# Kernel optimization log

Hardware: AMD Instinct MI355X
Metric: run time of the kernel (lower is better)

Reference implementation:

```python
import jax, jax.numpy as jnp
import numpy as np

N_NODES = 200000
D = 128            # in_channels
B_GRAPHS = 512     # batch_size
STEPS = 3          # processing_steps


def setup_inputs() -> dict:
    key = jax.random.key(0)
    k = jax.random.split(key, 6)
    x = jax.random.normal(k[0], (N_NODES, D), dtype=jnp.float32)
    batch = jnp.sort(jax.random.randint(k[1], (N_NODES,), 0, B_GRAPHS, dtype=jnp.int64))
    s = 0.1
    W_ih = jax.random.normal(k[2], (3 * D, 2 * D), dtype=jnp.float32) * s
    W_hh = jax.random.normal(k[3], (3 * D, D), dtype=jnp.float32) * s
    b_ih = jax.random.normal(k[4], (3 * D,), dtype=jnp.float32) * s
    b_hh = jax.random.normal(k[5], (3 * D,), dtype=jnp.float32) * s
    return {"x": x, "batch": batch, "batch_size": B_GRAPHS,
            "W_ih": W_ih, "W_hh": W_hh, "b_ih": b_ih, "b_hh": b_hh}


def _gru_cell(inp, h, W_ih, W_hh, b_ih, b_hh):
    # inp: [B, 2d], h: [B, d]; PyTorch GRU gate order: r, z, n
    gi = inp @ W_ih.T + b_ih  # [B, 3d]
    gh = h @ W_hh.T + b_hh    # [B, 3d]
    gi_r, gi_z, gi_n = jnp.split(gi, 3, axis=-1)
    gh_r, gh_z, gh_n = jnp.split(gh, 3, axis=-1)
    r = jax.nn.sigmoid(gi_r + gh_r)
    z = jax.nn.sigmoid(gi_z + gh_z)
    n = jnp.tanh(gi_n + r * gh_n)
    return (1.0 - z) * n + z * h


def reference(x, batch, batch_size, W_ih, W_hh, b_ih, b_hh):
    B = batch_size
    d = x.shape[1]
    h = jnp.zeros((B, d), dtype=x.dtype)
    q_star = jnp.zeros((B, 2 * d), dtype=x.dtype)
    for _ in range(STEPS):
        h = _gru_cell(q_star, h, W_ih, W_hh, b_ih, b_hh)
        q = h  # num_layers=1: output == new hidden state
        e = jnp.sum(x * q[batch], axis=-1)  # [N]
        m = jax.ops.segment_max(e, batch, num_segments=B)
        ex = jnp.exp(e - m[batch])
        s = jax.ops.segment_sum(ex, batch, num_segments=B)
        a = ex / (s[batch] + 1e-16)  # segment softmax weights [N]
        r = jax.ops.segment_sum(a[:, None] * x, batch, num_segments=B)  # [B, d]
        q_star = jnp.concatenate([q, r], axis=-1)
    return q_star
```

## Files before the change

### kernel.cpp

```cpp
#include <hip/hip_runtime.h>
#include <math.h>

constexpr int D = 128;
constexpr int B = 512;
constexpr int STEPS = 3;
constexpr int NW_IH = 3 * D * 2 * D;
constexpr int NW_HH = 3 * D * D;

__device__ __forceinline__ float sigmoidf_(float x) { return 1.f / (1.f + __expf(-x)); }
__device__ __forceinline__ float bflo(unsigned int u) { return __uint_as_float(u << 16); }
__device__ __forceinline__ float bfhi(unsigned int u) { return __uint_as_float(u & 0xffff0000u); }
__device__ __forceinline__ unsigned short f2bf_rn(float f) {
    unsigned int u = __float_as_uint(f);
    u += 0x7fffu + ((u >> 16) & 1u);
    return (unsigned short)(u >> 16);
}
__device__ __forceinline__ float4 ld4(const float* p) { return *(const float4*)p; }

__global__ __launch_bounds__(256) void k_prep(const float* __restrict__ Wih,
        const float* __restrict__ Whh, const int* __restrict__ batch, int n,
        unsigned short* __restrict__ wih_bf, unsigned short* __restrict__ whh_bf,
        int* __restrict__ seg) {
    int i = blockIdx.x * blockDim.x + threadIdx.x;
    if (i < NW_IH) wih_bf[i] = f2bf_rn(Wih[i]);
    else if (i < NW_IH + NW_HH) whh_bf[i - NW_IH] = f2bf_rn(Whh[i - NW_IH]);
    if (i <= B) {
        int lo = 0, hi = n;
        while (lo < hi) { int mid = (lo + hi) >> 1; if (batch[mid] < i) lo = mid + 1; else hi = mid; }
        seg[i] = lo;
    }
}

struct Trip { float4 a0, a1, b0, b1, c0, c1, d0, d1; };

__global__ __launch_bounds__(256, 2) void k_set2set(
        const float* __restrict__ x,
        const unsigned short* __restrict__ wih_bf,
        const unsigned short* __restrict__ whh_bf,
        const float* __restrict__ bih, const float* __restrict__ bhh,
        const int* __restrict__ seg, float* __restrict__ out) {
    __shared__ __align__(16) float s_q[2 * D];
    __shared__ __align__(16) float s_h[D];
    __shared__ float s_gi[3 * D], s_gh[3 * D];
    __shared__ float sm[16], sl[16];
    __shared__ __align__(16) float rpart[4][D];

    const int b = blockIdx.x;
    const int tid = threadIdx.x;
    const int start = seg[b], end = seg[b + 1];
    const int g = tid >> 4;
    const int s = tid & 15;

    if (tid < 2 * D) s_q[tid] = 0.f;
    if (tid < D) s_h[tid] = 0.f;
    __syncthreads();

    const int len = end - start;
    const int F = len >> 6;
    const float* xb = x + (size_t)(start + g) * D + s * 8;

    float m_run, l_run;
    float4 acc0, acc1;
    float4 q0, q1;

    auto load_trip = [&](Trip& T, int t) {
        const float* p = xb + (size_t)t * (64 * D);
        T.a0 = ld4(p);            T.a1 = ld4(p + 4);
        T.b0 = ld4(p + 16 * D);   T.b1 = ld4(p + 16 * D + 4);
        T.c0 = ld4(p + 32 * D);   T.c1 = ld4(p + 32 * D + 4);
        T.d0 = ld4(p + 48 * D);   T.d1 = ld4(p + 48 * D + 4);
    };
    auto dot8 = [&](const float4& lo, const float4& hi) {
        float p = lo.x * q0.x;
        p = fmaf(lo.y, q0.y, p); p = fmaf(lo.z, q0.z, p); p = fmaf(lo.w, q0.w, p);
        p = fmaf(hi.x, q1.x, p); p = fmaf(hi.y, q1.y, p);
        p = fmaf(hi.z, q1.z, p); p = fmaf(hi.w, q1.w, p);
        return p;
    };
    auto compute = [&](const Trip& T) {
        float p0 = dot8(T.a0, T.a1);
        float p1 = dot8(T.b0, T.b1);
        float p2 = dot8(T.c0, T.c1);
        float p3 = dot8(T.d0, T.d1);
        p0 += __shfl_xor(p0, 1, 64); p1 += __shfl_xor(p1, 1, 64);
        p2 += __shfl_xor(p2, 1, 64); p3 += __shfl_xor(p3, 1, 64);
        p0 += __shfl_xor(p0, 2, 64); p1 += __shfl_xor(p1, 2, 64);
        p2 += __shfl_xor(p2, 2, 64); p3 += __shfl_xor(p3, 2, 64);
        p0 += __shfl_xor(p0, 4, 64); p1 += __shfl_xor(p1, 4, 64);
        p2 += __shfl_xor(p2, 4, 64); p3 += __shfl_xor(p3, 4, 64);
        p0 += __shfl_xor(p0, 8, 64); p1 += __shfl_xor(p1, 8, 64);
        p2 += __shfl_xor(p2, 8, 64); p3 += __shfl_xor(p3, 8, 64);
        float nm = fmaxf(m_run, fmaxf(fmaxf(p0, p1), fmaxf(p2, p3)));
        float sc = __expf(m_run - nm);
        float e0 = __expf(p0 - nm), e1 = __expf(p1 - nm);
        float e2 = __expf(p2 - nm), e3 = __expf(p3 - nm);
        l_run = fmaf(l_run, sc, (e0 + e1) + (e2 + e3));
        acc0.x = fmaf(acc0.x, sc, fmaf(e0, T.a0.x, fmaf(e1, T.b0.x, fmaf(e2, T.c0.x, e3 * T.d0.x))));
        acc0.y = fmaf(acc0.y, sc, fmaf(e0, T.a0.y, fmaf(e1, T.b0.y, fmaf(e2, T.c0.y, e3 * T.d0.y))));
        acc0.z = fmaf(acc0.z, sc, fmaf(e0, T.a0.z, fmaf(e1, T.b0.z, fmaf(e2, T.c0.z, e3 * T.d0.z))));
        acc0.w = fmaf(acc0.w, sc, fmaf(e0, T.a0.w, fmaf(e1, T.b0.w, fmaf(e2, T.c0.w, e3 * T.d0.w))));
        acc1.x = fmaf(acc1.x, sc, fmaf(e0, T.a1.x, fmaf(e1, T.b1.x, fmaf(e2, T.c1.x, e3 * T.d1.x))));
        acc1.y = fmaf(acc1.y, sc, fmaf(e0, T.a1.y, fmaf(e1, T.b1.y, fmaf(e2, T.c1.y, e3 * T.d1.y))));
        acc1.z = fmaf(acc1.z, sc, fmaf(e0, T.a1.z, fmaf(e1, T.b1.z, fmaf(e2, T.c1.z, e3 * T.d1.z))));
        acc1.w = fmaf(acc1.w, sc, fmaf(e0, T.a1.w, fmaf(e1, T.b1.w, fmaf(e2, T.c1.w, e3 * T.d1.w))));
        m_run = nm;
    };
    auto one_node = [&](const float4& v0, const float4& v1) {
        float p = dot8(v0, v1);
        p += __shfl_xor(p, 1, 64);
        p += __shfl_xor(p, 2, 64);
        p += __shfl_xor(p, 4, 64);
        p += __shfl_xor(p, 8, 64);
        float nm = fmaxf(m_run, p);
        float sc = __expf(m_run - nm);
        float e  = __expf(p - nm);
        l_run = fmaf(l_run, sc, e);
        acc0.x = fmaf(acc0.x, sc, e * v0.x);
        acc0.y = fmaf(acc0.y, sc, e * v0.y);
        acc0.z = fmaf(acc0.z, sc, e * v0.z);
        acc0.w = fmaf(acc0.w, sc, e * v0.w);
        acc1.x = fmaf(acc1.x, sc, e * v1.x);
        acc1.y = fmaf(acc1.y, sc, e * v1.y);
        acc1.z = fmaf(acc1.z, sc, e * v1.z);
        acc1.w = fmaf(acc1.w, sc, e * v1.w);
        m_run = nm;
    };

    Trip A, Bv;

    for (int step = 0; step < STEPS; ++step) {
        if (F > 0) load_trip(A, 0);

        if (tid < 192) {
            const int r0 = tid * 2, r1 = r0 + 1;
            float gi0 = bih[r0], gi1 = bih[r1];
            float gh0 = bhh[r0], gh1 = bhh[r1];
            const float4* q4 = (const float4*)s_q;
            const float4* h4 = (const float4*)s_h;
            const uint4* w0 = (const uint4*)(wih_bf + (size_t)r0 * (2 * D));
            const uint4* w1 = (const uint4*)(wih_bf + (size_t)r1 * (2 * D));
#pragma unroll 4
            for (int c = 0; c < 32; ++c) {
                uint4 wa = w0[c], wb = w1[c];
                float4 qa = q4[2 * c], qb = q4[2 * c + 1];
                gi0 = fmaf(bflo(wa.x), qa.x, gi0); gi0 = fmaf(bfhi(wa.x), qa.y, gi0);
                gi0 = fmaf(bflo(wa.y), qa.z, gi0); gi0 = fmaf(bfhi(wa.y), qa.w, gi0);
                gi0 = fmaf(bflo(wa.z), qb.x, gi0); gi0 = fmaf(bfhi(wa.z), qb.y, gi0);
                gi0 = fmaf(bflo(wa.w), qb.z, gi0); gi0 = fmaf(bfhi(wa.w), qb.w, gi0);
                gi1 = fmaf(bflo(wb.x), qa.x, gi1); gi1 = fmaf(bfhi(wb.x), qa.y, gi1);
                gi1 = fmaf(bflo(wb.y), qa.z, gi1); gi1 = fmaf(bfhi(wb.y), qa.w, gi1);
                gi1 = fmaf(bflo(wb.z), qb.x, gi1); gi1 = fmaf(bfhi(wb.z), qb.y, gi1);
                gi1 = fmaf(bflo(wb.w), qb.z, gi1); gi1 = fmaf(bfhi(wb.w), qb.w, gi1);
            }
            const uint4* v0 = (const uint4*)(whh_bf + (size_t)r0 * D);
            const uint4* v1 = (const uint4*)(whh_bf + (size_t)r1 * D);
#pragma unroll 4
            for (int c = 0; c < 16; ++c) {
                uint4 wa = v0[c], wb = v1[c];
                float4 ha = h4[2 * c], hb = h4[2 * c + 1];
                gh0 = fmaf(bflo(wa.x), ha.x, gh0); gh0 = fmaf(bfhi(wa.x), ha.y, gh0);
                gh0 = fmaf(bflo(wa.y), ha.z, gh0); gh0 = fmaf(bfhi(wa.y), ha.w, gh0);
                gh0 = fmaf(bflo(wa.z), hb.x, gh0); gh0 = fmaf(bfhi(wa.z), hb.y, gh0);
                gh0 = fmaf(bflo(wa.w), hb.z, gh0); gh0 = fmaf(bfhi(wa.w), hb.w, gh0);
                gh1 = fmaf(bflo(wb.x), ha.x, gh1); gh1 = fmaf(bfhi(wb.x), ha.y, gh1);
                gh1 = fmaf(bflo(wb.y), ha.z, gh1); gh1 = fmaf(bfhi(wb.y), ha.w, gh1);
                gh1 = fmaf(bflo(wb.z), hb.x, gh1); gh1 = fmaf(bfhi(wb.z), hb.y, gh1);
                gh1 = fmaf(bflo(wb.w), hb.z, gh1); gh1 = fmaf(bfhi(wb.w), hb.w, gh1);
            }
            s_gi[r0] = gi0; s_gi[r1] = gi1;
            s_gh[r0] = gh0; s_gh[r1] = gh1;
        }
        __syncthreads();
        if (tid < D) {
            const int t = tid;
            float r  = sigmoidf_(s_gi[t] + s_gh[t]);
            float z  = sigmoidf_(s_gi[D + t] + s_gh[D + t]);
            float nn = tanhf(s_gi[2 * D + t] + r * s_gh[2 * D + t]);
            float hn = (1.f - z) * nn + z * s_h[t];
            s_h[t] = hn;
            s_q[t] = hn;
        }
        __syncthreads();

        q0 = ((const float4*)s_h)[2 * s];
        q1 = ((const float4*)s_h)[2 * s + 1];
        m_run = -INFINITY; l_run = 0.f;
        acc0 = make_float4(0.f, 0.f, 0.f, 0.f);
        acc1 = make_float4(0.f, 0.f, 0.f, 0.f);

        if (F > 0) {
            int t = 0;
            for (; t + 2 < F; t += 2) {
                load_trip(Bv, t + 1); compute(A);
                load_trip(A,  t + 2); compute(Bv);
            }
            if (t + 2 == F) { load_trip(Bv, t + 1); compute(A); compute(Bv); }
            else            { compute(A); }
        }
        {
            const int nt = start + g + (F << 6);
#pragma unroll
            for (int u = 0; u < 4; ++u) {
                const int nd = nt + (u << 4);
                if (nd < end) {
                    const float* p = x + (size_t)nd * D + s * 8;
                    one_node(ld4(p), ld4(p + 4));
                }
            }
        }

        if (s == 0) { sm[g] = m_run; sl[g] = l_run; }
        __syncthreads();

        {
            const float mv = sm[s];
            const float lv = sl[s];
            float M = mv;
            M = fmaxf(M, __shfl_xor(M, 1, 64));
            M = fmaxf(M, __shfl_xor(M, 2, 64));
            M = fmaxf(M, __shfl_xor(M, 4, 64));
            M = fmaxf(M, __shfl_xor(M, 8, 64));
            float term = (mv == -INFINITY) ? 0.f : lv * __expf(mv - M);
            term += __shfl_xor(term, 1, 64);
            term += __shfl_xor(term, 2, 64);
            term += __shfl_xor(term, 4, 64);
            term += __shfl_xor(term, 8, 64);
            const float inv = 1.f / (term + 1e-16f);
            const float fac = (m_run == -INFINITY) ? 0.f : __expf(m_run - M) * inv;
            acc0.x *= fac; acc0.y *= fac; acc0.z *= fac; acc0.w *= fac;
            acc1.x *= fac; acc1.y *= fac; acc1.z *= fac; acc1.w *= fac;
        }
        acc0.x += __shfl_xor(acc0.x, 16, 64); acc0.y += __shfl_xor(acc0.y, 16, 64);
        acc0.z += __shfl_xor(acc0.z, 16, 64); acc0.w += __shfl_xor(acc0.w, 16, 64);
        acc1.x += __shfl_xor(acc1.x, 16, 64); acc1.y += __shfl_xor(acc1.y, 16, 64);
        acc1.z += __shfl_xor(acc1.z, 16, 64); acc1.w += __shfl_xor(acc1.w, 16, 64);
        acc0.x += __shfl_xor(acc0.x, 32, 64); acc0.y += __shfl_xor(acc0.y, 32, 64);
        acc0.z += __shfl_xor(acc0.z, 32, 64); acc0.w += __shfl_xor(acc0.w, 32, 64);
        acc1.x += __shfl_xor(acc1.x, 32, 64); acc1.y += __shfl_xor(acc1.y, 32, 64);
        acc1.z += __shfl_xor(acc1.z, 32, 64); acc1.w += __shfl_xor(acc1.w, 32, 64);

        const int wv = tid >> 6;
        if ((tid & 63) < 16) {
            float4* dst = (float4*)&rpart[wv][s * 8];
            dst[0] = acc0; dst[1] = acc1;
        }
        __syncthreads();
        if (tid < D) {
            float v = (rpart[0][tid] + rpart[1][tid]) + (rpart[2][tid] + rpart[3][tid]);
            s_q[D + tid] = v;
        }
        __syncthreads();
    }

    if (tid < 2 * D) out[(size_t)b * (2 * D) + tid] = s_q[tid];
}

extern "C" void kernel_launch(void* const* d_in, const int* in_sizes, int n_in,
                              void* d_out, int out_size, void* d_ws, size_t ws_size,
                              hipStream_t stream) {
    const float* x    = (const float*)d_in[0];
    const int*   batch= (const int*)d_in[1];
    const float* Wih  = (const float*)d_in[3];
    const float* Whh  = (const float*)d_in[4];
    const float* bih  = (const float*)d_in[5];
    const float* bhh  = (const float*)d_in[6];
    const int n = in_sizes[0] / D;

    char* ws = (char*)d_ws;
    int* seg = (int*)ws;
    unsigned short* wih_bf = (unsigned short*)(ws + 4096);
    unsigned short* whh_bf = (unsigned short*)(ws + 4096 + (size_t)NW_IH * 2);

    const int total = NW_IH + NW_HH;
    k_prep<<<(total + 255) / 256, 256, 0, stream>>>(Wih, Whh, batch, n, wih_bf, whh_bf, seg);
    k_set2set<<<B, 256, 0, stream>>>(x, wih_bf, whh_bf, bih, bhh, seg, (float*)d_out);
}
```

Before: 236.2 us.

## Deepen x prefetch to four trips and overlap next-step loads with reductions

The streaming loop now keeps four trips of x rows in registers instead of two, and handles the segment tail with clamped loads plus masking instead of a separate per-node loop. The first four trips for the next step are issued before the cross-group reduction and the GRU matvec, so their memory latency is hidden behind that work. A finite sentinel replaces -INFINITY so the special-case checks can be dropped. This costs many more live vector registers, which under launch_bounds(256,2) could cause spills or lower occupancy.

```diff
diff --git a/kernel.cpp b/kernel.cpp
--- a/kernel.cpp
+++ b/kernel.cpp
@@ -1,11 +1,13 @@
 #include <hip/hip_runtime.h>
 #include <math.h>
+#include <float.h>
 
 constexpr int D = 128;
 constexpr int B = 512;
 constexpr int STEPS = 3;
 constexpr int NW_IH = 3 * D * 2 * D;
 constexpr int NW_HH = 3 * D * D;
+constexpr float NEG_HUGE = -3.402823466e38f;
 
 __device__ __forceinline__ float sigmoidf_(float x) { return 1.f / (1.f + __expf(-x)); }
 __device__ __forceinline__ float bflo(unsigned int u) { return __uint_as_float(u << 16); }
@@ -16,6 +18,7 @@
     return (unsigned short)(u >> 16);
 }
 __device__ __forceinline__ float4 ld4(const float* p) { return *(const float4*)p; }
+__device__ __forceinline__ int imin_(int a, int b) { return a < b ? a : b; }
 
 __global__ __launch_bounds__(256) void k_prep(const float* __restrict__ Wih,
         const float* __restrict__ Whh, const int* __restrict__ batch, int n,
@@ -50,25 +53,28 @@
     const int start = seg[b], end = seg[b + 1];
     const int g = tid >> 4;
     const int s = tid & 15;
-
-    if (tid < 2 * D) s_q[tid] = 0.f;
-    if (tid < D) s_h[tid] = 0.f;
-    __syncthreads();
+    const int s8 = s * 8;
 
     const int len = end - start;
-    const int F = len >> 6;
-    const float* xb = x + (size_t)(start + g) * D + s * 8;
+    const int FT = (len + 63) >> 6;
+    const int gbase = start + g;
+    const int eclamp = (len > 0) ? end - 1 : start;
 
     float m_run, l_run;
     float4 acc0, acc1;
     float4 q0, q1;
+    Trip T0_, T1_, T2_, T3_;
 
     auto load_trip = [&](Trip& T, int t) {
-        const float* p = xb + (size_t)t * (64 * D);
-        T.a0 = ld4(p);            T.a1 = ld4(p + 4);
-        T.b0 = ld4(p + 16 * D);   T.b1 = ld4(p + 16 * D + 4);
-        T.c0 = ld4(p + 32 * D);   T.c1 = ld4(p + 32 * D + 4);
-        T.d0 = ld4(p + 48 * D);   T.d1 = ld4(p + 48 * D + 4);
+        const int n0 = gbase + (t << 6);
+        const float* p0 = x + ((size_t)imin_(n0,      eclamp) << 7) + s8;
+        const float* p1 = x + ((size_t)imin_(n0 + 16, eclamp) << 7) + s8;
+        const float* p2 = x + ((size_t)imin_(n0 + 32, eclamp) << 7) + s8;
+        const float* p3 = x + ((size_t)imin_(n0 + 48, eclamp) << 7) + s8;
+        T.a0 = ld4(p0); T.a1 = ld4(p0 + 4);
+        T.b0 = ld4(p1); T.b1 = ld4(p1 + 4);
+        T.c0 = ld4(p2); T.c1 = ld4(p2 + 4);
+        T.d0 = ld4(p3); T.d1 = ld4(p3 + 4);
     };
     auto dot8 = [&](const float4& lo, const float4& hi) {
         float p = lo.x * q0.x;
@@ -77,7 +83,7 @@
         p = fmaf(hi.z, q1.z, p); p = fmaf(hi.w, q1.w, p);
         return p;
     };
-    auto compute = [&](const Trip& T) {
+    auto compute_core = [&](const Trip& T, bool masked, int t) {
         float p0 = dot8(T.a0, T.a1);
         float p1 = dot8(T.b0, T.b1);
         float p2 = dot8(T.c0, T.c1);
@@ -90,10 +96,22 @@
         p2 += __shfl_xor(p2, 4, 64); p3 += __shfl_xor(p3, 4, 64);
         p0 += __shfl_xor(p0, 8, 64); p1 += __shfl_xor(p1, 8, 64);
         p2 += __shfl_xor(p2, 8, 64); p3 += __shfl_xor(p3, 8, 64);
-        float nm = fmaxf(m_run, fmaxf(fmaxf(p0, p1), fmaxf(p2, p3)));
+        bool m0 = true, m1 = true, m2 = true, m3 = true;
+        float h0 = p0, h1 = p1, h2 = p2, h3 = p3;
+        if (masked) {
+            const int n0 = gbase + (t << 6);
+            m0 = n0 < end; m1 = n0 + 16 < end; m2 = n0 + 32 < end; m3 = n0 + 48 < end;
+            h0 = m0 ? p0 : NEG_HUGE; h1 = m1 ? p1 : NEG_HUGE;
+            h2 = m2 ? p2 : NEG_HUGE; h3 = m3 ? p3 : NEG_HUGE;
+        }
+        float nm = fmaxf(m_run, fmaxf(fmaxf(h0, h1), fmaxf(h2, h3)));
         float sc = __expf(m_run - nm);
         float e0 = __expf(p0 - nm), e1 = __expf(p1 - nm);
         float e2 = __expf(p2 - nm), e3 = __expf(p3 - nm);
+        if (masked) {
+            e0 = m0 ? e0 : 0.f; e1 = m1 ? e1 : 0.f;
+            e2 = m2 ? e2 : 0.f; e3 = m3 ? e3 : 0.f;
+        }
         l_run = fmaf(l_run, sc, (e0 + e1) + (e2 + e3));
         acc0.x = fmaf(acc0.x, sc, fmaf(e0, T.a0.x, fmaf(e1, T.b0.x, fmaf(e2, T.c0.x, e3 * T.d0.x))));
         acc0.y = fmaf(acc0.y, sc, fmaf(e0, T.a0.y, fmaf(e1, T.b0.y, fmaf(e2, T.c0.y, e3 * T.d0.y))));
@@ -105,32 +123,19 @@
         acc1.w = fmaf(acc1.w, sc, fmaf(e0, T.a1.w, fmaf(e1, T.b1.w, fmaf(e2, T.c1.w, e3 * T.d1.w))));
         m_run = nm;
     };
-    auto one_node = [&](const float4& v0, const float4& v1) {
-        float p = dot8(v0, v1);
-        p += __shfl_xor(p, 1, 64);
-        p += __shfl_xor(p, 2, 64);
-        p += __shfl_xor(p, 4, 64);
-        p += __shfl_xor(p, 8, 64);
-        float nm = fmaxf(m_run, p);
-        float sc = __expf(m_run - nm);
-        float e  = __expf(p - nm);
-        l_run = fmaf(l_run, sc, e);
-        acc0.x = fmaf(acc0.x, sc, e * v0.x);
-        acc0.y = fmaf(acc0.y, sc, e * v0.y);
-        acc0.z = fmaf(acc0.z, sc, e * v0.z);
-        acc0.w = fmaf(acc0.w, sc, e * v0.w);
-        acc1.x = fmaf(acc1.x, sc, e * v1.x);
-        acc1.y = fmaf(acc1.y, sc, e * v1.y);
-        acc1.z = fmaf(acc1.z, sc, e * v1.z);
-        acc1.w = fmaf(acc1.w, sc, e * v1.w);
-        m_run = nm;
-    };
-
-    Trip A, Bv;
+    auto compute  = [&](const Trip& T)        { compute_core(T, false, 0); };
+    auto computeM = [&](const Trip& T, int t) { compute_core(T, true,  t); };
+
+    if (FT > 0) load_trip(T0_, 0);
+    if (FT > 1) load_trip(T1_, 1);
+    if (FT > 2) load_trip(T2_, 2);
+    if (FT > 3) load_trip(T3_, 3);
+
+    if (tid < 2 * D) s_q[tid] = 0.f;
+    if (tid < D) s_h[tid] = 0.f;
+    __syncthreads();
 
     for (int step = 0; step < STEPS; ++step) {
-        if (F > 0) load_trip(A, 0);
-
         if (tid < 192) {
             const int r0 = tid * 2, r1 = r0 + 1;
             float gi0 = bih[r0], gi1 = bih[r1];
@@ -184,29 +189,36 @@
 
         q0 = ((const float4*)s_h)[2 * s];
         q1 = ((const float4*)s_h)[2 * s + 1];
-        m_run = -INFINITY; l_run = 0.f;
+        m_run = NEG_HUGE; l_run = 0.f;
         acc0 = make_float4(0.f, 0.f, 0.f, 0.f);
         acc1 = make_float4(0.f, 0.f, 0.f, 0.f);
 
-        if (F > 0) {
-            int t = 0;
-            for (; t + 2 < F; t += 2) {
-                load_trip(Bv, t + 1); compute(A);
-                load_trip(A,  t + 2); compute(Bv);
-            }
-            if (t + 2 == F) { load_trip(Bv, t + 1); compute(A); compute(Bv); }
-            else            { compute(A); }
-        }
-        {
-            const int nt = start + g + (F << 6);
-#pragma unroll
-            for (int u = 0; u < 4; ++u) {
-                const int nd = nt + (u << 4);
-                if (nd < end) {
-                    const float* p = x + (size_t)nd * D + s * 8;
-                    one_node(ld4(p), ld4(p + 4));
-                }
-            }
+        int t = 0;
+        while (t + 8 <= FT) {
+            compute(T0_); load_trip(T0_, t + 4);
+            compute(T1_); load_trip(T1_, t + 5);
+            compute(T2_); load_trip(T2_, t + 6);
+            compute(T3_); load_trip(T3_, t + 7);
+            t += 4;
+        }
+        int rem = FT - t;
+        if (rem > 4) {
+            compute(T0_); load_trip(T0_, t + 4);
+            compute(T1_); if (rem > 5) load_trip(T1_, t + 5);
+            compute(T2_); if (rem > 6) load_trip(T2_, t + 6);
+            compute(T3_);
+            t += 4; rem -= 4;
+        }
+        if (rem > 0) { if (t     == FT - 1) computeM(T0_, t);     else compute(T0_); }
+        if (rem > 1) { if (t + 1 == FT - 1) computeM(T1_, t + 1); else compute(T1_); }
+        if (rem > 2) { if (t + 2 == FT - 1) computeM(T2_, t + 2); else compute(T2_); }
+        if (rem > 3) computeM(T3_, t + 3);
+
+        if (step + 1 < STEPS) {
+            if (FT > 0) load_trip(T0_, 0);
+            if (FT > 1) load_trip(T1_, 1);
+            if (FT > 2) load_trip(T2_, 2);
+            if (FT > 3) load_trip(T3_, 3);
         }
 
         if (s == 0) { sm[g] = m_run; sl[g] = l_run; }
@@ -220,13 +232,13 @@
             M = fmaxf(M, __shfl_xor(M, 2, 64));
             M = fmaxf(M, __shfl_xor(M, 4, 64));
             M = fmaxf(M, __shfl_xor(M, 8, 64));
-            float term = (mv == -INFINITY) ? 0.f : lv * __expf(mv - M);
+            float term = lv * __expf(mv - M);
             term += __shfl_xor(term, 1, 64);
             term += __shfl_xor(term, 2, 64);
             term += __shfl_xor(term, 4, 64);
             term += __shfl_xor(term, 8, 64);
             const float inv = 1.f / (term + 1e-16f);
-            const float fac = (m_run == -INFINITY) ? 0.f : __expf(m_run - M) * inv;
+            const float fac = __expf(m_run - M) * inv;
             acc0.x *= fac; acc0.y *= fac; acc0.z *= fac; acc0.w *= fac;
             acc1.x *= fac; acc1.y *= fac; acc1.z *= fac; acc1.w *= fac;
         }
@@ -241,7 +253,7 @@
 
         const int wv = tid >> 6;
         if ((tid & 63) < 16) {
-            float4* dst = (float4*)&rpart[wv][s * 8];
+            float4* dst = (float4*)&rpart[wv][s8];
             dst[0] = acc0; dst[1] = acc1;
         }
         __syncthreads();
```

New measurement: 268.3 us. +13.6%, slower.
